# Kernel optimization log

Hardware: AMD Instinct MI355X
Metric: run time of the kernel (lower is better)

Reference implementation:

```python
import math
import jax, jax.numpy as jnp
import numpy as np

N_HEADS = 16
D_EMBED = 1024
D_HEAD = D_EMBED // N_HEADS


def setup_inputs() -> dict:
    key = jax.random.key(0)
    k1, k2, k3, k4, k5 = jax.random.split(key, 5)
    B, S, D = 4, 2048, D_EMBED
    scale = 1.0 / math.sqrt(D)
    return {
        "x": jax.random.normal(k1, (B, S, D), dtype=jnp.float32),
        "in_proj_w": jax.random.normal(k2, (3 * D, D), dtype=jnp.float32) * scale,
        "in_proj_b": jax.random.normal(k3, (3 * D,), dtype=jnp.float32) * 0.02,
        "out_proj_w": jax.random.normal(k4, (D, D), dtype=jnp.float32) * scale,
        "out_proj_b": jax.random.normal(k5, (D,), dtype=jnp.float32) * 0.02,
        "causal_mask": 0,
    }


def reference(x, in_proj_w, in_proj_b, out_proj_w, out_proj_b, causal_mask):
    B, S, D = x.shape
    # in_proj: torch Linear -> x @ W^T + b, then chunk into q,k,v
    qkv = x @ in_proj_w.T + in_proj_b              # [B,S,3D]
    q, k, v = jnp.split(qkv, 3, axis=-1)
    # [B,S,D] -> [B,H,S,d]
    def heads(t):
        return t.reshape(B, S, N_HEADS, D_HEAD).transpose(0, 2, 1, 3)
    q, k, v = heads(q), heads(k), heads(v)
    weight = jnp.einsum("bhsd,bhtd->bhst", q, k)   # [B,H,S,S] materialized scores
    if causal_mask:
        mask = jnp.triu(jnp.ones((S, S), dtype=bool), k=1)
        weight = jnp.where(mask, -jnp.inf, weight)
    weight = jax.nn.softmax(weight / math.sqrt(D_HEAD), axis=-1)
    out = jnp.einsum("bhst,bhtd->bhsd", weight, v)  # [B,H,S,d]
    out = out.transpose(0, 2, 1, 3).reshape(B, S, D)
    return out @ out_proj_w.T + out_proj_b
```

## Files before the change

kernel.cpp:

```cpp
#include <hip/hip_runtime.h>

typedef unsigned short u16;
typedef _Float16 h8 __attribute__((ext_vector_type(8)));
typedef __fp16 fp16x2 __attribute__((ext_vector_type(2)));
typedef float f32x4 __attribute__((ext_vector_type(4)));

constexpr int B_ = 4, S_ = 2048, D_ = 1024, H_ = 16;

__device__ __forceinline__ void async16(const void* g, void* l) {
  __builtin_amdgcn_global_load_lds(
      (const __attribute__((address_space(1))) void*)g,
      (__attribute__((address_space(3))) void*)l, 16, 0, 0);
}

__device__ __forceinline__ unsigned pk2(float a, float b) {
  union { fp16x2 h; unsigned u; } c;
  c.h = __builtin_amdgcn_cvt_pkrtz(a, b);
  return c.u;
}

__device__ __forceinline__ float fexp2(float x) {
#if __has_builtin(__builtin_amdgcn_exp2f)
  return __builtin_amdgcn_exp2f(x);
#else
  return exp2f(x);
#endif
}

#define QSCALE 0.18033688011112042f

__global__ __launch_bounds__(256) void cvt3_kernel(
    const float* __restrict__ x, const float* __restrict__ wi,
    const float* __restrict__ wo, _Float16* __restrict__ xh,
    _Float16* __restrict__ wih, _Float16* __restrict__ woh)
{
  const int bid = blockIdx.x;
  const float* src;
  _Float16* dst;
  int base;
  if (bid < 8192)       { src = x;  dst = xh;  base = bid; }
  else if (bid < 11264) { src = wi; dst = wih; base = bid - 8192; }
  else                  { src = wo; dst = woh; base = bid - 11264; }
  const int i = (base * 256 + threadIdx.x) * 4;
  const float4 v = *(const float4*)(src + i);
  uint2 o;
  o.x = pk2(v.x, v.y);
  o.y = pk2(v.z, v.w);
  *(uint2*)(dst + i) = o;
}

template<bool OUT_HALF, int BPW, bool SCALE_Q>
__global__ __launch_bounds__(512, 2) void gemm256d_f16(
    const _Float16* __restrict__ A, const _Float16* __restrict__ Bw,
    const float* __restrict__ bias, void* __restrict__ Cout,
    int M, int N, int K)
{
  constexpr int BN = BPW * 64;
  constexpr int NBB = BN / 8;
  __shared__ __align__(16) _Float16 sA[2][16384];
  __shared__ __align__(16) _Float16 sB[2][NBB * 512];

  const int tid = threadIdx.x;
  const int lane = tid & 63, w = tid >> 6;
  const int wm = w >> 2, wn = w & 3;

  const int id = blockIdx.x;
  const int cpx = gridDim.x >> 3;
  const int swz = (id & 7) * cpx + (id >> 3);
  const int nbx = N / BN;
  const int bx = swz % nbx, by = swz / nbx;
  const int m0 = by * 256, n0 = bx * BN;

  const int r15 = lane & 15, s4 = lane >> 4;
  const _Float16* gA[4];
  int loA[4];
#pragma unroll
  for (int j = 0; j < 4; ++j) {
    const int t = 2 * w + (j >> 1), kk = j & 1;
    gA[j] = A + (size_t)(m0 + 16 * t + r15) * K + kk * 32 + s4 * 8;
    loA[j] = (t * 2 + kk) * 512;
  }
  const _Float16* gB[BPW];
  int loB[BPW];
#pragma unroll
  for (int j = 0; j < BPW; ++j) {
    const int f = w * BPW + j, nt = f >> 1, kk = f & 1;
    gB[j] = Bw + (size_t)(n0 + 16 * nt + r15) * K + kk * 32 + s4 * 8;
    loB[j] = f * 512;
  }

  const f32x4 zf = {0.f, 0.f, 0.f, 0.f};
  f32x4 acc[8][BPW];
#pragma unroll
  for (int i = 0; i < 8; ++i)
#pragma unroll
    for (int j = 0; j < BPW; ++j) acc[i][j] = zf;

#pragma unroll
  for (int j = 0; j < 4; ++j) async16(gA[j], &sA[0][loA[j]]);
#pragma unroll
  for (int j = 0; j < BPW; ++j) async16(gB[j], &sB[0][loB[j]]);
#pragma unroll
  for (int j = 0; j < 4; ++j) async16(gA[j] + 64, &sA[1][loA[j]]);
#pragma unroll
  for (int j = 0; j < BPW; ++j) async16(gB[j] + 64, &sB[1][loB[j]]);
  if constexpr (BPW == 2)      asm volatile("s_waitcnt vmcnt(6)" ::: "memory");
  else if constexpr (BPW == 3) asm volatile("s_waitcnt vmcnt(7)" ::: "memory");
  else                         asm volatile("s_waitcnt vmcnt(8)" ::: "memory");
  __builtin_amdgcn_s_barrier();

  const int NT = K >> 6;
  int cur = 0;
  for (int kt = 0; kt < NT; ++kt) {
    const _Float16* pA = sA[cur];
    const _Float16* pB = sB[cur];
    _Float16* nA = sA[cur];
    _Float16* nB = sB[cur];
    const bool st = (kt + 2 < NT);
    const int ko = (kt + 2) * 64;

    h8 fb[BPW][2];
#pragma unroll
    for (int p = 0; p < 4; ++p) {
      if (p == 0) {
#pragma unroll
        for (int nt = 0; nt < BPW; ++nt)
#pragma unroll
          for (int kk = 0; kk < 2; ++kk)
            fb[nt][kk] = *(const h8*)&pB[((wn * BPW + nt) * 2 + kk) * 512 + lane * 8];
      } else if (st) {
        if (p == 1) {
#pragma unroll
          for (int j = 0; j < BPW; ++j) async16(gB[j] + ko, &nB[loB[j]]);
        }
        if ((w & 3) == p - 1) {
#pragma unroll
          for (int j = 0; j < 4; ++j) async16(gA[j] + ko, &nA[loA[j]]);
        }
      }
      h8 fa[2][2];
#pragma unroll
      for (int i = 0; i < 2; ++i)
#pragma unroll
        for (int kk = 0; kk < 2; ++kk)
          fa[i][kk] = *(const h8*)&pA[((wm * 8 + 2 * p + i) * 2 + kk) * 512 + lane * 8];
      __builtin_amdgcn_s_setprio(1);
#pragma unroll
      for (int i = 0; i < 2; ++i)
#pragma unroll
        for (int nt = 0; nt < BPW; ++nt)
#pragma unroll
          for (int kk = 0; kk < 2; ++kk)
            acc[2 * p + i][nt] = __builtin_amdgcn_mfma_f32_16x16x32_f16(
                fa[i][kk], fb[nt][kk], acc[2 * p + i][nt], 0, 0, 0);
      __builtin_amdgcn_s_setprio(0);
      __builtin_amdgcn_s_barrier();
    }
    if (st && (w & 3) == 3) {
#pragma unroll
      for (int j = 0; j < 4; ++j) async16(gA[j] + ko, &nA[loA[j]]);
    }
    if (kt + 1 < NT) {
      if (st) {
        if constexpr (BPW == 2)      asm volatile("s_waitcnt vmcnt(6)" ::: "memory");
        else if constexpr (BPW == 3) asm volatile("s_waitcnt vmcnt(7)" ::: "memory");
        else                         asm volatile("s_waitcnt vmcnt(8)" ::: "memory");
      } else {
        asm volatile("s_waitcnt vmcnt(0)" ::: "memory");
      }
      __builtin_amdgcn_s_barrier();
    }
    cur ^= 1;
  }

  const int g = lane >> 4, cc = lane & 15;
#pragma unroll
  for (int nt = 0; nt < BPW; ++nt) {
    const int col = n0 + wn * (16 * BPW) + nt * 16 + cc;
    const float bv = bias[col];
    float qs = 1.0f;
    if constexpr (SCALE_Q) qs = (col < 1024) ? QSCALE : 1.0f;
#pragma unroll
    for (int mt = 0; mt < 8; ++mt) {
      const int rowb = m0 + wm * 128 + mt * 16 + g * 4;
#pragma unroll
      for (int r = 0; r < 4; ++r) {
        float v = acc[mt][nt][r] + bv;
        if constexpr (SCALE_Q) v *= qs;
        if constexpr (OUT_HALF)
          ((_Float16*)Cout)[(size_t)(rowb + r) * N + col] = (_Float16)v;
        else
          ((float*)Cout)[(size_t)(rowb + r) * N + col] = v;
      }
    }
  }
}

__global__ __launch_bounds__(256) void transpose_v(
    const u16* __restrict__ qkv, u16* __restrict__ vT)
{
  __shared__ u16 T[64 * 73];
  const int tid = threadIdx.x;
  const int bh = blockIdx.y, s0 = blockIdx.x * 64;
  const int b = bh >> 4, h = bh & 15;
#pragma unroll
  for (int t = 0; t < 2; ++t) {
    const int c = tid + t * 256, r = c >> 3, cs = c & 7;
    union { int4 v; u16 s[8]; } u;
    u.v = *(const int4*)(qkv + (size_t)(b * S_ + s0 + r) * 3072 + 2048 + h * 64 + 8 * cs);
#pragma unroll
    for (int i = 0; i < 8; ++i) T[r * 73 + 8 * cs + i] = u.s[i];
  }
  __syncthreads();
#pragma unroll
  for (int t = 0; t < 2; ++t) {
    const int c = tid + t * 256, rd = c >> 3, ss = c & 7;
    union { int4 v; u16 s[8]; } u;
#pragma unroll
    for (int i = 0; i < 8; ++i) u.s[i] = T[(8 * ss + i) * 73 + rd];
    *(int4*)(vT + (size_t)(bh * 64 + rd) * S_ + s0 + 8 * ss) = u.v;
  }
}

__global__ __launch_bounds__(256, 4) void attn_f16(
    const _Float16* __restrict__ qkv, const _Float16* __restrict__ vT,
    _Float16* __restrict__ attnO, const int* __restrict__ causal_ptr)
{
  __shared__ __align__(16) _Float16 sQP[9216];
  __shared__ __align__(16) _Float16 sK[4096];
  __shared__ __align__(16) _Float16 sV[4096];

  const int tid = threadIdx.x, lane = tid & 63, w = tid >> 6;
  const int q4 = lane >> 4, cc = lane & 15;
  const int bh = blockIdx.y, b = bh >> 4, h = bh & 15;
  const int q0 = blockIdx.x * 128;
  const int causal = causal_ptr[0];

  {
    const int rr = lane & 15, sc8 = lane >> 4;
#pragma unroll
    for (int tt = 0; tt < 2; ++tt) {
      const int t = 2 * w + tt;
#pragma unroll
      for (int sh = 0; sh < 2; ++sh) {
        const _Float16* g = qkv + (size_t)(b * S_ + q0 + 16 * t + rr) * 3072 + h * 64 + 8 * (4 * sh + sc8);
        async16(g, &sQP[t * 1024 + sh * 512]);
      }
    }
  }
  __syncthreads();

  h8 qf[2][2];
#pragma unroll
  for (int m = 0; m < 2; ++m)
#pragma unroll
    for (int kk = 0; kk < 2; ++kk)
      qf[m][kk] = *(const h8*)&sQP[((2 * w + m) << 10) + (kk << 9) + (lane << 3)];

  h8 ones;
#pragma unroll
  for (int i = 0; i < 8; ++i) ones[i] = (_Float16)1.0f;

  const _Float16* gK = qkv + (size_t)(b * S_ + 16 * w + (lane & 15)) * 3072 + 1024 + h * 64 + 8 * (lane >> 4);
  const _Float16* gV = vT + (size_t)(bh * 64 + 16 * w + (lane & 15)) * S_ + 8 * (lane >> 4);
  _Float16* lK0 = &sK[w * 1024];
  _Float16* lV0 = &sV[w * 1024];

  const int wp = w * 2304;

  const f32x4 zf = {0.f, 0.f, 0.f, 0.f};
  f32x4 oa[2][4], lac[2];
#pragma unroll
  for (int m = 0; m < 2; ++m) {
    lac[m] = zf;
#pragma unroll
    for (int nt = 0; nt < 4; ++nt) oa[m][nt] = zf;
  }

  for (int j0 = 0; j0 < S_; j0 += 64) {
    if (causal && j0 > q0 + 127) break;
    __syncthreads();
    async16(gK + (size_t)j0 * 3072, lK0);
    async16(gK + (size_t)j0 * 3072 + 32, lK0 + 512);
    async16(gV + j0, lV0);
    async16(gV + j0 + 32, lV0 + 512);
    __syncthreads();

    f32x4 sc[2][4];
    __builtin_amdgcn_s_setprio(1);
#pragma unroll
    for (int nt = 0; nt < 4; ++nt) {
      const h8 kf0 = *(const h8*)&sK[(nt << 10) + (lane << 3)];
      const h8 kf1 = *(const h8*)&sK[(nt << 10) + 512 + (lane << 3)];
#pragma unroll
      for (int m = 0; m < 2; ++m) {
        sc[m][nt] = __builtin_amdgcn_mfma_f32_16x16x32_f16(kf0, qf[m][0], zf, 0, 0, 0);
        sc[m][nt] = __builtin_amdgcn_mfma_f32_16x16x32_f16(kf1, qf[m][1], sc[m][nt], 0, 0, 0);
      }
    }
    __builtin_amdgcn_s_setprio(0);

    if (causal) {
#pragma unroll
      for (int m = 0; m < 2; ++m)
#pragma unroll
        for (int nt = 0; nt < 4; ++nt)
#pragma unroll
          for (int r = 0; r < 4; ++r)
            if ((j0 + nt * 16 + q4 * 4 + r) > (q0 + 32 * w + m * 16 + cc))
              sc[m][nt][r] = -1.0e30f;
    }

#pragma unroll
    for (int m = 0; m < 2; ++m)
#pragma unroll
      for (int nt = 0; nt < 4; ++nt) {
        uint2 pk;
        pk.x = pk2(fexp2(sc[m][nt][0]), fexp2(sc[m][nt][1]));
        pk.y = pk2(fexp2(sc[m][nt][2]), fexp2(sc[m][nt][3]));
        *(uint2*)&sQP[wp + (m * 16 + cc) * 72 + nt * 16 + q4 * 4] = pk;
      }

    asm volatile("s_waitcnt lgkmcnt(0)" ::: "memory");

    h8 pf[2][2];
#pragma unroll
    for (int m = 0; m < 2; ++m)
#pragma unroll
      for (int kk = 0; kk < 2; ++kk)
        pf[m][kk] = *(const h8*)&sQP[wp + (m * 16 + cc) * 72 + kk * 32 + q4 * 8];

    __builtin_amdgcn_s_setprio(1);
#pragma unroll
    for (int m = 0; m < 2; ++m) {
      lac[m] = __builtin_amdgcn_mfma_f32_16x16x32_f16(pf[m][0], ones, lac[m], 0, 0, 0);
      lac[m] = __builtin_amdgcn_mfma_f32_16x16x32_f16(pf[m][1], ones, lac[m], 0, 0, 0);
    }
#pragma unroll
    for (int nt = 0; nt < 4; ++nt) {
      const h8 vf0 = *(const h8*)&sV[(nt << 10) + (lane << 3)];
      const h8 vf1 = *(const h8*)&sV[(nt << 10) + 512 + (lane << 3)];
#pragma unroll
      for (int m = 0; m < 2; ++m) {
        oa[m][nt] = __builtin_amdgcn_mfma_f32_16x16x32_f16(pf[m][0], vf0, oa[m][nt], 0, 0, 0);
        oa[m][nt] = __builtin_amdgcn_mfma_f32_16x16x32_f16(pf[m][1], vf1, oa[m][nt], 0, 0, 0);
      }
    }
    __builtin_amdgcn_s_setprio(0);
  }

#pragma unroll
  for (int m = 0; m < 2; ++m) {
    float inv[4];
#pragma unroll
    for (int r = 0; r < 4; ++r) inv[r] = 1.0f / lac[m][r];
#pragma unroll
    for (int nt = 0; nt < 4; ++nt) {
      const int col = h * 64 + nt * 16 + cc;
#pragma unroll
      for (int r = 0; r < 4; ++r) {
        const int row = b * S_ + q0 + 32 * w + m * 16 + q4 * 4 + r;
        attnO[(size_t)row * D_ + col] = (_Float16)(oa[m][nt][r] * inv[r]);
      }
    }
  }
}

extern "C" void kernel_launch(void* const* d_in, const int* in_sizes, int n_in,
                              void* d_out, int out_size, void* d_ws, size_t ws_size,
                              hipStream_t stream)
{
  const float* x  = (const float*)d_in[0];
  const float* wi = (const float*)d_in[1];
  const float* bi = (const float*)d_in[2];
  const float* wo = (const float*)d_in[3];
  const float* bo = (const float*)d_in[4];
  const int* causal = (const int*)d_in[5];

  _Float16* xh   = (_Float16*)d_ws;
  _Float16* wih  = xh + 8388608;
  _Float16* woh  = wih + 3145728;
  _Float16* qkvb = woh + 1048576;
  _Float16* vT   = qkvb + 25165824;
  _Float16* attn = vT + 8388608;

  const int M = B_ * S_;

  cvt3_kernel<<<12288, 256, 0, stream>>>(x, wi, wo, xh, wih, woh);

  gemm256d_f16<true, 3, true><<<512, 512, 0, stream>>>(
      xh, wih, bi, qkvb, M, 3 * D_, D_);

  transpose_v<<<dim3(32, 64), 256, 0, stream>>>((const u16*)qkvb, (u16*)vT);

  attn_f16<<<dim3(16, 64), 256, 0, stream>>>(qkvb, vT, attn, causal);

  gemm256d_f16<false, 2, false><<<256, 512, 0, stream>>>(
      attn, woh, bo, d_out, M, D_, D_);
}
```

Measured before the change: 311.7 us.

## Fuse V transpose into QKV GEMM epilogue and restructure GEMM k-loop pipeline

The QKV projection GEMM now writes the V columns directly into a transposed [B,H,d,S] buffer from its epilogue, which removes the separate transpose_v kernel and its extra read/write pass over V. The GEMM main loop is manually software-pipelined: all A fragments for the next phase are read before the current MFMA batch, and each phase is gated by explicit lgkmcnt waits and barriers, with B prefetch loads issued earlier. The attention kernel switches to a 1D grid with an XCD-style swizzle of block ids. The transposed V stores are 8-byte scattered writes with an S stride, which may be less coalesced than the old transpose's output.

```diff
diff --git a/kernel.cpp b/kernel.cpp
--- a/kernel.cpp
+++ b/kernel.cpp
@@ -28,6 +28,9 @@
 }
 
 #define QSCALE 0.18033688011112042f
+
+#define LGKM0 asm volatile("s_waitcnt lgkmcnt(0)" ::: "memory")
+#define FENCE asm volatile("" ::: "memory")
 
 __global__ __launch_bounds__(256) void cvt3_kernel(
     const float* __restrict__ x, const float* __restrict__ wi,
@@ -49,10 +52,11 @@
   *(uint2*)(dst + i) = o;
 }
 
-template<bool OUT_HALF, int BPW, bool SCALE_Q>
-__global__ __launch_bounds__(512, 2) void gemm256d_f16(
+template<bool OUT_HALF, int BPW, bool SCALE_Q, bool FUSE_V>
+__global__ __launch_bounds__(512, 2) void gemm256r_f16(
     const _Float16* __restrict__ A, const _Float16* __restrict__ Bw,
     const float* __restrict__ bias, void* __restrict__ Cout,
+    _Float16* __restrict__ vTout,
     int M, int N, int K)
 {
   constexpr int BN = BPW * 64;
@@ -97,17 +101,37 @@
     for (int j = 0; j < BPW; ++j) acc[i][j] = zf;
 
 #pragma unroll
+  for (int j = 0; j < BPW; ++j) async16(gB[j], &sB[0][loB[j]]);
+#pragma unroll
   for (int j = 0; j < 4; ++j) async16(gA[j], &sA[0][loA[j]]);
 #pragma unroll
-  for (int j = 0; j < BPW; ++j) async16(gB[j], &sB[0][loB[j]]);
+  for (int j = 0; j < BPW; ++j) async16(gB[j] + 64, &sB[1][loB[j]]);
 #pragma unroll
   for (int j = 0; j < 4; ++j) async16(gA[j] + 64, &sA[1][loA[j]]);
-#pragma unroll
-  for (int j = 0; j < BPW; ++j) async16(gB[j] + 64, &sB[1][loB[j]]);
   if constexpr (BPW == 2)      asm volatile("s_waitcnt vmcnt(6)" ::: "memory");
   else if constexpr (BPW == 3) asm volatile("s_waitcnt vmcnt(7)" ::: "memory");
   else                         asm volatile("s_waitcnt vmcnt(8)" ::: "memory");
   __builtin_amdgcn_s_barrier();
+  FENCE;
+
+#define RD_FA(dst, p)                                                        \
+  _Pragma("unroll")                                                          \
+  for (int i = 0; i < 2; ++i)                                                \
+    _Pragma("unroll")                                                        \
+    for (int kk = 0; kk < 2; ++kk)                                           \
+      dst[i][kk] = *(const h8*)&pA[((wm * 8 + 2 * (p) + i) * 2 + kk) * 512 + lane * 8];
+
+#define DO_MFMA(fa, p)                                                       \
+  __builtin_amdgcn_s_setprio(1);                                             \
+  _Pragma("unroll")                                                          \
+  for (int i = 0; i < 2; ++i)                                                \
+    _Pragma("unroll")                                                        \
+    for (int nt = 0; nt < BPW; ++nt)                                         \
+      _Pragma("unroll")                                                      \
+      for (int kk = 0; kk < 2; ++kk)                                         \
+        acc[2 * (p) + i][nt] = __builtin_amdgcn_mfma_f32_16x16x32_f16(       \
+            fa[i][kk], fb[nt][kk], acc[2 * (p) + i][nt], 0, 0, 0);           \
+  __builtin_amdgcn_s_setprio(0);
 
   const int NT = K >> 6;
   int cur = 0;
@@ -121,45 +145,56 @@
 
     h8 fb[BPW][2];
 #pragma unroll
-    for (int p = 0; p < 4; ++p) {
-      if (p == 0) {
-#pragma unroll
-        for (int nt = 0; nt < BPW; ++nt)
-#pragma unroll
-          for (int kk = 0; kk < 2; ++kk)
-            fb[nt][kk] = *(const h8*)&pB[((wn * BPW + nt) * 2 + kk) * 512 + lane * 8];
-      } else if (st) {
-        if (p == 1) {
-#pragma unroll
-          for (int j = 0; j < BPW; ++j) async16(gB[j] + ko, &nB[loB[j]]);
-        }
-        if ((w & 3) == p - 1) {
-#pragma unroll
-          for (int j = 0; j < 4; ++j) async16(gA[j] + ko, &nA[loA[j]]);
-        }
-      }
-      h8 fa[2][2];
-#pragma unroll
-      for (int i = 0; i < 2; ++i)
-#pragma unroll
-        for (int kk = 0; kk < 2; ++kk)
-          fa[i][kk] = *(const h8*)&pA[((wm * 8 + 2 * p + i) * 2 + kk) * 512 + lane * 8];
-      __builtin_amdgcn_s_setprio(1);
-#pragma unroll
-      for (int i = 0; i < 2; ++i)
-#pragma unroll
-        for (int nt = 0; nt < BPW; ++nt)
-#pragma unroll
-          for (int kk = 0; kk < 2; ++kk)
-            acc[2 * p + i][nt] = __builtin_amdgcn_mfma_f32_16x16x32_f16(
-                fa[i][kk], fb[nt][kk], acc[2 * p + i][nt], 0, 0, 0);
-      __builtin_amdgcn_s_setprio(0);
-      __builtin_amdgcn_s_barrier();
-    }
+    for (int nt = 0; nt < BPW; ++nt)
+#pragma unroll
+      for (int kk = 0; kk < 2; ++kk)
+        fb[nt][kk] = *(const h8*)&pB[((wn * BPW + nt) * 2 + kk) * 512 + lane * 8];
+    h8 fa0[2][2], fa1[2][2];
+    RD_FA(fa0, 0);
+    RD_FA(fa1, 1);
+
+    DO_MFMA(fa0, 0);
+    LGKM0;
+    __builtin_amdgcn_s_barrier();
+    FENCE;
+
+    h8 fa2[2][2];
+    RD_FA(fa2, 2);
+    if (st) {
+#pragma unroll
+      for (int j = 0; j < BPW; ++j) async16(gB[j] + ko, &nB[loB[j]]);
+      if ((w & 3) == 0) {
+#pragma unroll
+        for (int j = 0; j < 4; ++j) async16(gA[j] + ko, &nA[loA[j]]);
+      }
+    }
+    DO_MFMA(fa1, 1);
+    LGKM0;
+    __builtin_amdgcn_s_barrier();
+    FENCE;
+
+    h8 fa3[2][2];
+    RD_FA(fa3, 3);
+    if (st && (w & 3) == 1) {
+#pragma unroll
+      for (int j = 0; j < 4; ++j) async16(gA[j] + ko, &nA[loA[j]]);
+    }
+    DO_MFMA(fa2, 2);
+    LGKM0;
+    __builtin_amdgcn_s_barrier();
+    FENCE;
+
+    if (st && (w & 3) == 2) {
+#pragma unroll
+      for (int j = 0; j < 4; ++j) async16(gA[j] + ko, &nA[loA[j]]);
+    }
+    DO_MFMA(fa3, 3);
+    LGKM0;
     if (st && (w & 3) == 3) {
 #pragma unroll
       for (int j = 0; j < 4; ++j) async16(gA[j] + ko, &nA[loA[j]]);
     }
+
     if (kt + 1 < NT) {
       if (st) {
         if constexpr (BPW == 2)      asm volatile("s_waitcnt vmcnt(6)" ::: "memory");
@@ -169,9 +204,12 @@
         asm volatile("s_waitcnt vmcnt(0)" ::: "memory");
       }
       __builtin_amdgcn_s_barrier();
+      FENCE;
     }
     cur ^= 1;
   }
+#undef RD_FA
+#undef DO_MFMA
 
   const int g = lane >> 4, cc = lane & 15;
 #pragma unroll
@@ -183,42 +221,29 @@
 #pragma unroll
     for (int mt = 0; mt < 8; ++mt) {
       const int rowb = m0 + wm * 128 + mt * 16 + g * 4;
+      float vv[4];
 #pragma unroll
       for (int r = 0; r < 4; ++r) {
-        float v = acc[mt][nt][r] + bv;
-        if constexpr (SCALE_Q) v *= qs;
-        if constexpr (OUT_HALF)
-          ((_Float16*)Cout)[(size_t)(rowb + r) * N + col] = (_Float16)v;
-        else
-          ((float*)Cout)[(size_t)(rowb + r) * N + col] = v;
-      }
-    }
-  }
-}
-
-__global__ __launch_bounds__(256) void transpose_v(
-    const u16* __restrict__ qkv, u16* __restrict__ vT)
-{
-  __shared__ u16 T[64 * 73];
-  const int tid = threadIdx.x;
-  const int bh = blockIdx.y, s0 = blockIdx.x * 64;
-  const int b = bh >> 4, h = bh & 15;
-#pragma unroll
-  for (int t = 0; t < 2; ++t) {
-    const int c = tid + t * 256, r = c >> 3, cs = c & 7;
-    union { int4 v; u16 s[8]; } u;
-    u.v = *(const int4*)(qkv + (size_t)(b * S_ + s0 + r) * 3072 + 2048 + h * 64 + 8 * cs);
-#pragma unroll
-    for (int i = 0; i < 8; ++i) T[r * 73 + 8 * cs + i] = u.s[i];
-  }
-  __syncthreads();
-#pragma unroll
-  for (int t = 0; t < 2; ++t) {
-    const int c = tid + t * 256, rd = c >> 3, ss = c & 7;
-    union { int4 v; u16 s[8]; } u;
-#pragma unroll
-    for (int i = 0; i < 8; ++i) u.s[i] = T[(8 * ss + i) * 73 + rd];
-    *(int4*)(vT + (size_t)(bh * 64 + rd) * S_ + s0 + 8 * ss) = u.v;
+        vv[r] = acc[mt][nt][r] + bv;
+        if constexpr (SCALE_Q) vv[r] *= qs;
+      }
+      bool vcol = false;
+      if constexpr (FUSE_V) vcol = (col >= 2048);
+      if (vcol) {
+        union { _Float16 hx[4]; uint2 u; } pv;
+#pragma unroll
+        for (int r = 0; r < 4; ++r) pv.hx[r] = (_Float16)vv[r];
+        *(uint2*)&vTout[((size_t)(((rowb >> 11) << 10) + (col - 2048)) << 11) + (rowb & 2047)] = pv.u;
+      } else {
+#pragma unroll
+        for (int r = 0; r < 4; ++r) {
+          if constexpr (OUT_HALF)
+            ((_Float16*)Cout)[(size_t)(rowb + r) * N + col] = (_Float16)vv[r];
+          else
+            ((float*)Cout)[(size_t)(rowb + r) * N + col] = vv[r];
+        }
+      }
+    }
   }
 }
 
@@ -232,8 +257,10 @@
 
   const int tid = threadIdx.x, lane = tid & 63, w = tid >> 6;
   const int q4 = lane >> 4, cc = lane & 15;
-  const int bh = blockIdx.y, b = bh >> 4, h = bh & 15;
-  const int q0 = blockIdx.x * 128;
+  const int id = blockIdx.x;
+  const int swz = (id & 7) * 128 + (id >> 3);
+  const int bh = swz >> 4, b = bh >> 4, h = bh & 15;
+  const int q0 = (swz & 15) << 7;
   const int causal = causal_ptr[0];
 
   {
@@ -321,7 +348,7 @@
         *(uint2*)&sQP[wp + (m * 16 + cc) * 72 + nt * 16 + q4 * 4] = pk;
       }
 
-    asm volatile("s_waitcnt lgkmcnt(0)" ::: "memory");
+    LGKM0;
 
     h8 pf[2][2];
 #pragma unroll
@@ -388,13 +415,11 @@
 
   cvt3_kernel<<<12288, 256, 0, stream>>>(x, wi, wo, xh, wih, woh);
 
-  gemm256d_f16<true, 3, true><<<512, 512, 0, stream>>>(
-      xh, wih, bi, qkvb, M, 3 * D_, D_);
-
-  transpose_v<<<dim3(32, 64), 256, 0, stream>>>((const u16*)qkvb, (u16*)vT);
-
-  attn_f16<<<dim3(16, 64), 256, 0, stream>>>(qkvb, vT, attn, causal);
-
-  gemm256d_f16<false, 2, false><<<256, 512, 0, stream>>>(
-      attn, woh, bo, d_out, M, D_, D_);
-}
+  gemm256r_f16<true, 3, true, true><<<512, 512, 0, stream>>>(
+      xh, wih, bi, qkvb, vT, M, 3 * D_, D_);
+
+  attn_f16<<<1024, 256, 0, stream>>>(qkvb, vT, attn, causal);
+
+  gemm256r_f16<false, 2, false, false><<<256, 512, 0, stream>>>(
+      attn, woh, bo, d_out, nullptr, M, D_, D_);
+}
```

After: 296.0 us. 5.0% less time.
